# Kernel optimization log

Measured on AMD Instinct MI355X. Metric: run time of the kernel, lower is better.

## Reference

```python
import jax, jax.numpy as jnp
import numpy as np

N = 50000          # nodes
DEG = 16           # out-degree
E = N * DEG        # edges
IN = 256           # input feature dim
H = 8              # hidden heads
DH = 32            # per-head hidden dim (hidden_dim // H)
HID = H * DH       # 256
OUT = 64           # output dim (single output head)
ALPHA = 0.2        # LeakyReLU negative slope


def _xavier(k, shape, fan_in, fan_out):
    limit = 1.414 * np.sqrt(6.0 / (fan_in + fan_out))
    return jax.random.uniform(k, shape, jnp.float32, -limit, limit)


def setup_inputs() -> dict:
    key = jax.random.key(0)
    ks = jax.random.split(key, 6)
    X = jax.random.normal(ks[0], (N, IN), jnp.float32)
    src = jnp.repeat(jnp.arange(N, dtype=jnp.int32), DEG)      # every row non-empty
    dst = jax.random.randint(ks[1], (E,), 0, N, jnp.int32)
    edges = jnp.stack([src, dst])                               # [2, E]
    W0 = _xavier(ks[2], (H, IN, DH), IN, DH)
    a0 = _xavier(ks[3], (H, 2 * DH), 2 * DH, 1)
    W1 = _xavier(ks[4], (1, HID, OUT), HID, OUT)
    a1 = _xavier(ks[5], (1, 2 * OUT), 2 * OUT, 1)
    return {"X": X, "edges": edges, "W0": W0, "a0": a0, "W1": W1, "a1": a1}


def sparse_gat_layer(X, edges, W, a):
    # W: [H, Din, D], a: [H, 2D]. Equivalent to concat(h_src, h_dst) @ a split.
    n = X.shape[0]
    D = W.shape[2]
    src, dst = edges[0], edges[1]
    h = jnp.einsum('nd,hde->hne', X, W)                         # [H, N, D]
    s_src = jnp.einsum('hne,he->hn', h, a[:, :D])               # [H, N]
    s_dst = jnp.einsum('hne,he->hn', h, a[:, D:])               # [H, N]
    e = jax.nn.leaky_relu(s_src[:, src] + s_dst[:, dst], ALPHA)  # [H, E]
    # stable per-row (segment = src) softmax, matching torch.sparse.softmax(dim=1)
    seg_max = jax.lax.stop_gradient(
        jax.vmap(lambda v: jax.ops.segment_max(v, src, num_segments=n))(e))
    p = jnp.exp(e - seg_max[:, src])
    denom = jax.vmap(lambda v: jax.ops.segment_sum(v, src, num_segments=n))(p)
    att = p / denom[:, src]                                      # [H, E]
    # out[i] = sum_{e: src=i} att_e * h[dst_e]
    agg = jax.vmap(lambda a_, hh: jax.ops.segment_sum(a_[:, None] * hh[dst], src,
                                                      num_segments=n))(att, h)
    return agg                                                   # [H, N, D]


def reference(X, edges, W0, a0, W1, a1):
    h1 = jax.nn.elu(sparse_gat_layer(X, edges, W0, a0))          # [H, N, DH]
    X1 = jnp.transpose(h1, (1, 0, 2)).reshape(X.shape[0], -1)    # concat heads [N, HID]
    out = sparse_gat_layer(X1, edges, W1, a1)                    # [1, N, OUT]
    return jax.nn.elu(out[0])                                    # num_heads_out = 1
```

## Files before the change

### kernel.cpp

```cpp
#include <hip/hip_runtime.h>

typedef __attribute__((ext_vector_type(8))) short bh8;
typedef __attribute__((ext_vector_type(4))) float f4;

static __device__ __forceinline__ float b2f(unsigned short u){
  union { unsigned int i; float f; } c; c.i = ((unsigned int)u) << 16; return c.f;
}
static __device__ __forceinline__ unsigned short f2b(float f){
  union { float f; unsigned int i; } c; c.f = f;
  unsigned int u = c.i; u += 0x7fffu + ((u >> 16) & 1u);
  return (unsigned short)(u >> 16);
}
static __device__ __forceinline__ float elu1(float x){ return x > 0.f ? x : (__expf(x) - 1.f); }
static __device__ __forceinline__ float lrelu(float x){ return x > 0.f ? x : 0.2f * x; }
static __device__ __forceinline__ float gload(const void* p, size_t i, int isf32){
  return isf32 ? ((const float*)p)[i] : b2f(((const unsigned short*)p)[i]);
}
static __device__ __forceinline__ int detect_f32(const unsigned int* __restrict__ W0w, int lane){
  unsigned int w = W0w[lane & 63];
  unsigned int e = (w >> 7) & 0xFFu;
  unsigned long long m = __ballot(e >= 100u && e <= 126u);
  return (__popcll(m) < 32) ? 1 : 0;
}

__global__ __launch_bounds__(256) void prep_kernel(
    const void* __restrict__ W0, const void* __restrict__ a0,
    const void* __restrict__ W1, const void* __restrict__ a1,
    unsigned short* __restrict__ Wt1, unsigned short* __restrict__ Wt2){
  int isf = detect_f32((const unsigned int*)W0, threadIdx.x & 63);
  int c = blockIdx.x, k = threadIdx.x;
  if (c < 272){
    float v;
    if (c < 256){
      int h = c >> 5, d = c & 31;
      v = gload(W0, (size_t)(h*256 + k)*32 + d, isf);
    } else if (c < 264){
      int h = c - 256; float s = 0.f;
      for (int d = 0; d < 32; d++)
        s += gload(W0, (size_t)(h*256 + k)*32 + d, isf) * gload(a0, h*64 + d, isf);
      v = s;
    } else {
      int h = c - 264; float s = 0.f;
      for (int d = 0; d < 32; d++)
        s += gload(W0, (size_t)(h*256 + k)*32 + d, isf) * gload(a0, h*64 + 32 + d, isf);
      v = s;
    }
    Wt1[c*256 + k] = f2b(v);
  } else {
    int c2 = c - 272; float v;
    if (c2 < 64) v = gload(W1, k*64 + c2, isf);
    else if (c2 == 64){ float s = 0.f; for (int i = 0; i < 64; i++) s += gload(W1, k*64+i, isf) * gload(a1, i, isf);      v = s; }
    else if (c2 == 65){ float s = 0.f; for (int i = 0; i < 64; i++) s += gload(W1, k*64+i, isf) * gload(a1, 64 + i, isf); v = s; }
    else v = 0.f;
    Wt2[c2*256 + k] = f2b(v);
  }
}

__global__ __launch_bounds__(256, 2) void gemm1_mfma(
    const void* __restrict__ Xraw, const unsigned short* __restrict__ Wt,
    unsigned short* __restrict__ H1, float* __restrict__ S1, int N,
    const void* __restrict__ W0){
  __shared__ __align__(16) unsigned short A[112*264];
  int tid = threadIdx.x, wv = tid >> 6, lane = tid & 63;
  int isf = detect_f32((const unsigned int*)W0, lane);
  int q = lane >> 4, l = lane & 15;
  int n0 = blockIdx.x*112;
  #pragma unroll
  for (int it = 0; it < 14; it++){
    int g = it*256 + tid;
    int r = g >> 5, c = g & 31;
    int grow = n0 + r; if (grow > N-1) grow = N-1;
    bh8 v;
    if (isf){
      const float* xr = (const float*)Xraw + (size_t)grow*256 + c*8;
      float4 u0 = *(const float4*)xr, u1 = *(const float4*)(xr + 4);
      v[0]=(short)f2b(u0.x); v[1]=(short)f2b(u0.y); v[2]=(short)f2b(u0.z); v[3]=(short)f2b(u0.w);
      v[4]=(short)f2b(u1.x); v[5]=(short)f2b(u1.y); v[6]=(short)f2b(u1.z); v[7]=(short)f2b(u1.w);
    } else {
      v = *(const bh8*)((const unsigned short*)Xraw + (size_t)grow*256 + c*8);
    }
    *(bh8*)&A[r*264 + c*8] = v;
  }
  __syncthreads();
  const bh8* Wb = (const bh8*)Wt;
  bh8 B[4][8];
  #pragma unroll
  for (int tt = 0; tt < 4; tt++){
    int t = wv*4 + tt;
    #pragma unroll
    for (int kk = 0; kk < 8; kk++) B[tt][kk] = Wb[(size_t)(t*16 + l)*32 + kk*4 + q];
  }
  for (int m = 0; m < 7; m++){
    bh8 a[8];
    #pragma unroll
    for (int kk = 0; kk < 8; kk++) a[kk] = *(const bh8*)&A[(m*16 + l)*264 + kk*32 + q*8];
    #pragma unroll
    for (int tt = 0; tt < 4; tt++){
      f4 acc = {0.f,0.f,0.f,0.f};
      #pragma unroll
      for (int kk = 0; kk < 8; kk++)
        acc = __builtin_amdgcn_mfma_f32_16x16x32_bf16(a[kk], B[tt][kk], acc, 0, 0, 0);
      int t = wv*4 + tt;
      #pragma unroll
      for (int r = 0; r < 4; r++){
        int row = n0 + m*16 + q*4 + r;
        if (row < N) H1[(size_t)row*256 + t*16 + l] = f2b(acc[r]);
      }
    }
  }
  if (wv == 0){
    bh8 Bs[8];
    #pragma unroll
    for (int kk = 0; kk < 8; kk++) Bs[kk] = Wb[(size_t)(256 + l)*32 + kk*4 + q];
    for (int m = 0; m < 7; m++){
      bh8 a[8];
      #pragma unroll
      for (int kk = 0; kk < 8; kk++) a[kk] = *(const bh8*)&A[(m*16 + l)*264 + kk*32 + q*8];
      f4 acc = {0.f,0.f,0.f,0.f};
      #pragma unroll
      for (int kk = 0; kk < 8; kk++)
        acc = __builtin_amdgcn_mfma_f32_16x16x32_bf16(a[kk], Bs[kk], acc, 0, 0, 0);
      #pragma unroll
      for (int r = 0; r < 4; r++){
        int row = n0 + m*16 + q*4 + r;
        if (row < N) S1[(size_t)row*16 + l] = acc[r];
      }
    }
  }
}

__global__ __launch_bounds__(256) void fused_agg1_gemm2(
    const float* __restrict__ S1, const unsigned short* __restrict__ H1,
    const int* __restrict__ dst, const unsigned short* __restrict__ Wt2,
    unsigned short* __restrict__ H2, float* __restrict__ S2, int N){
  __shared__ __align__(16) unsigned short Xt[32*264];
  __shared__ __align__(16) unsigned short Hs[32*88];
  int tid = threadIdx.x, wv = tid >> 6, lane = tid & 63;
  int n0 = blockIdx.x*32;
  int h = lane >> 3, jj = lane & 7;
  int half = lane >> 5, li = lane & 31;
  int cb = li*8, hc = li >> 2;
  for (int np = 0; np < 4; np++){
    int lrA = wv*8 + np*2, lrB = lrA + 1;
    int nodeA = n0 + lrA; if (nodeA > N-1) nodeA = N-1;
    int nodeB = n0 + lrB; if (nodeB > N-1) nodeB = N-1;
    const int* dpA = dst + (size_t)nodeA*16;
    const int* dpB = dst + (size_t)nodeB*16;
    int d0A = dpA[jj], d1A = dpA[jj + 8];
    int d0B = dpB[jj], d1B = dpB[jj + 8];
    float ssA = S1[(size_t)nodeA*16 + h];
    float ssB = S1[(size_t)nodeB*16 + h];
    float e0A = lrelu(ssA + S1[(size_t)d0A*16 + 8 + h]);
    float e1A = lrelu(ssA + S1[(size_t)d1A*16 + 8 + h]);
    float e0B = lrelu(ssB + S1[(size_t)d0B*16 + 8 + h]);
    float e1B = lrelu(ssB + S1[(size_t)d1B*16 + 8 + h]);
    float mA = fmaxf(e0A, e1A), mB = fmaxf(e0B, e1B);
    mA = fmaxf(mA, __shfl_xor(mA, 1)); mB = fmaxf(mB, __shfl_xor(mB, 1));
    mA = fmaxf(mA, __shfl_xor(mA, 2)); mB = fmaxf(mB, __shfl_xor(mB, 2));
    mA = fmaxf(mA, __shfl_xor(mA, 4)); mB = fmaxf(mB, __shfl_xor(mB, 4));
    float p0A = __expf(e0A - mA), p1A = __expf(e1A - mA);
    float p0B = __expf(e0B - mB), p1B = __expf(e1B - mB);
    float sA = p0A + p1A, sB = p0B + p1B;
    sA += __shfl_xor(sA, 1); sB += __shfl_xor(sB, 1);
    sA += __shfl_xor(sA, 2); sB += __shfl_xor(sB, 2);
    sA += __shfl_xor(sA, 4); sB += __shfl_xor(sB, 4);
    float invA = 1.f / sA, invB = 1.f / sB;
    float v0A = p0A * invA, v1A = p1A * invA;
    float v0B = p0B * invB, v1B = p1B * invB;
    float accA[8] = {0.f,0.f,0.f,0.f,0.f,0.f,0.f,0.f};
    float accB[8] = {0.f,0.f,0.f,0.f,0.f,0.f,0.f,0.f};
    #pragma unroll
    for (int i = 0; i < 8; i++){
      int j  = i*2 + half;
      int jl = j & 7;
      int rowA  = (i < 4) ? __shfl(d0A, jl) : __shfl(d1A, jl);
      int rowB  = (i < 4) ? __shfl(d0B, jl) : __shfl(d1B, jl);
      float awA = (i < 4) ? __shfl(v0A, hc*8 + jl) : __shfl(v1A, hc*8 + jl);
      float awB = (i < 4) ? __shfl(v0B, hc*8 + jl) : __shfl(v1B, hc*8 + jl);
      bh8 vA = *(const bh8*)(H1 + (size_t)rowA*256 + cb);
      bh8 vB = *(const bh8*)(H1 + (size_t)rowB*256 + cb);
      #pragma unroll
      for (int c = 0; c < 8; c++){
        accA[c] += awA * b2f((unsigned short)vA[c]);
        accB[c] += awB * b2f((unsigned short)vB[c]);
      }
    }
    #pragma unroll
    for (int c = 0; c < 8; c++){
      accA[c] += __shfl_xor(accA[c], 32);
      accB[c] += __shfl_xor(accB[c], 32);
    }
    if (half == 0){
      bh8 oA, oB;
      #pragma unroll
      for (int c = 0; c < 8; c++){
        oA[c] = (short)f2b(elu1(accA[c]));
        oB[c] = (short)f2b(elu1(accB[c]));
      }
      *(bh8*)&Xt[lrA*264 + cb] = oA;
      *(bh8*)&Xt[lrB*264 + cb] = oB;
    }
  }
  __syncthreads();
  {
    int q = lane >> 4, l = lane & 15;
    bh8 a0[8], a1[8];
    #pragma unroll
    for (int kk = 0; kk < 8; kk++){
      a0[kk] = *(const bh8*)&Xt[l*264 + kk*32 + q*8];
      a1[kk] = *(const bh8*)&Xt[(16 + l)*264 + kk*32 + q*8];
    }
    const bh8* Wb = (const bh8*)Wt2;
    int ntt = (wv == 3) ? 2 : 1;
    for (int it = 0; it < ntt; it++){
      int tt = (it == 0) ? wv : 4;
      bh8 b[8];
      #pragma unroll
      for (int kk = 0; kk < 8; kk++) b[kk] = Wb[(size_t)(tt*16 + l)*32 + kk*4 + q];
      f4 c0 = {0.f,0.f,0.f,0.f}, c1 = {0.f,0.f,0.f,0.f};
      #pragma unroll
      for (int kk = 0; kk < 8; kk++){
        c0 = __builtin_amdgcn_mfma_f32_16x16x32_bf16(a0[kk], b[kk], c0, 0, 0, 0);
        c1 = __builtin_amdgcn_mfma_f32_16x16x32_bf16(a1[kk], b[kk], c1, 0, 0, 0);
      }
      if (tt < 4){
        #pragma unroll
        for (int r = 0; r < 4; r++){
          Hs[(q*4 + r)*88 + tt*16 + l]      = f2b(c0[r]);
          Hs[(16 + q*4 + r)*88 + tt*16 + l] = f2b(c1[r]);
        }
      } else if (l < 2){
        #pragma unroll
        for (int r = 0; r < 4; r++){
          int row0 = n0 + q*4 + r, row1 = n0 + 16 + q*4 + r;
          if (row0 < N) S2[(size_t)row0*2 + l] = c0[r];
          if (row1 < N) S2[(size_t)row1*2 + l] = c1[r];
        }
      }
    }
  }
  __syncthreads();
  {
    int r2 = tid >> 3, ch = tid & 7;
    int row = n0 + r2;
    if (row < N)
      *(bh8*)(H2 + (size_t)row*64 + ch*8) = *(const bh8*)&Hs[r2*88 + ch*8];
  }
}

__global__ __launch_bounds__(256) void agg2_kernel(
    const float* __restrict__ S2, const unsigned short* __restrict__ H2,
    const int* __restrict__ dst, void* __restrict__ outv, int N,
    const void* __restrict__ W0){
  int tid = threadIdx.x, wv = tid >> 6, lane = tid & 63;
  int isf = detect_f32((const unsigned int*)W0, lane);
  int node = blockIdx.x*4 + wv; if (node > N-1) node = N-1;
  int j = lane & 15;
  int d = dst[(size_t)node*16 + j];
  float e = lrelu(S2[(size_t)node*2] + S2[(size_t)d*2 + 1]);
  float m = e;
  m = fmaxf(m, __shfl_xor(m, 1)); m = fmaxf(m, __shfl_xor(m, 2));
  m = fmaxf(m, __shfl_xor(m, 4)); m = fmaxf(m, __shfl_xor(m, 8));
  float p = __expf(e - m);
  float s = p;
  s += __shfl_xor(s, 1); s += __shfl_xor(s, 2); s += __shfl_xor(s, 4); s += __shfl_xor(s, 8);
  float attv = p / s;
  int g = lane >> 3, cbl = (lane & 7)*8;
  float acc[8] = {0.f,0.f,0.f,0.f,0.f,0.f,0.f,0.f};
  #pragma unroll
  for (int it = 0; it < 2; it++){
    int j2 = it*8 + g;
    float aw = __shfl(attv, j2);
    int row  = __shfl(d,    j2);
    bh8 v = *(const bh8*)(H2 + (size_t)row*64 + cbl);
    #pragma unroll
    for (int c = 0; c < 8; c++) acc[c] += aw * b2f((unsigned short)v[c]);
  }
  #pragma unroll
  for (int c = 0; c < 8; c++){
    acc[c] += __shfl_xor(acc[c], 8);
    acc[c] += __shfl_xor(acc[c], 16);
    acc[c] += __shfl_xor(acc[c], 32);
  }
  if (lane < 8){
    size_t oi = (size_t)node*64 + cbl;
    if (isf){
      float4 f0, f1;
      f0.x = elu1(acc[0]); f0.y = elu1(acc[1]); f0.z = elu1(acc[2]); f0.w = elu1(acc[3]);
      f1.x = elu1(acc[4]); f1.y = elu1(acc[5]); f1.z = elu1(acc[6]); f1.w = elu1(acc[7]);
      *(float4*)((float*)outv + oi)     = f0;
      *(float4*)((float*)outv + oi + 4) = f1;
    } else {
      bh8 o;
      #pragma unroll
      for (int c = 0; c < 8; c++) o[c] = (short)f2b(elu1(acc[c]));
      *(bh8*)((unsigned short*)outv + oi) = o;
    }
  }
}

extern "C" void kernel_launch(void* const* d_in, const int* in_sizes, int n_in,
                              void* d_out, int out_size, void* d_ws, size_t ws_size,
                              hipStream_t stream){
  const void* X  = d_in[0];
  const int*  ed = (const int*)d_in[1];
  const void* W0 = d_in[2];
  const void* a0 = d_in[3];
  const void* W1 = d_in[4];
  const void* a1 = d_in[5];

  int N = in_sizes[0] / 256;
  int E = N * 16;
  const int* dst = ed + E;

  char* w = (char*)d_ws;
  size_t off = 0;
  auto alloc = [&](size_t bytes) -> void* {
    void* p = w + off; off += (bytes + 255) & ~(size_t)255; return p;
  };
  unsigned short* Wt1 = (unsigned short*)alloc(272*256*2);
  unsigned short* Wt2 = (unsigned short*)alloc(80*256*2);
  float*          S1  = (float*)alloc((size_t)N*16*4);
  unsigned short* H1  = (unsigned short*)alloc((size_t)N*256*2);
  unsigned short* H2  = (unsigned short*)alloc((size_t)N*64*2);
  float*          S2  = (float*)alloc((size_t)N*2*4);
  (void)ws_size; (void)n_in; (void)out_size;

  int g1 = (N + 111) / 112;
  int gf = (N + 31) / 32;
  int ab = (N + 3) / 4;
  prep_kernel     <<<352,256, 0, stream>>>(W0, a0, W1, a1, Wt1, Wt2);
  gemm1_mfma      <<<g1, 256, 0, stream>>>(X,  Wt1, H1, S1, N, W0);
  fused_agg1_gemm2<<<gf, 256, 0, stream>>>(S1, H1, dst, Wt2, H2, S2, N);
  agg2_kernel     <<<ab, 256, 0, stream>>>(S2, H2, dst, d_out, N, W0);
}
```

Before: 218.4 us.

## Stage GEMM1 output in LDS for coalesced stores; process two nodes per wave in agg2

In gemm1, the per-element scattered 2-byte stores of H1 are replaced by writing MFMA results back into the shared A tile (after the A fragments are consumed) and then emitting coalesced 16-byte row stores. The separate score-GEMM pass for wave 0 is folded into the main m loop, which reuses the loaded A fragments. agg2 now handles two nodes per wave with interleaved gathers to raise memory-level parallelism, and its grid is halved. The added __syncthreads per m iteration and the extra live registers are the costs.

```diff
diff --git a/kernel.cpp b/kernel.cpp
--- a/kernel.cpp
+++ b/kernel.cpp
@@ -90,42 +90,51 @@
     #pragma unroll
     for (int kk = 0; kk < 8; kk++) B[tt][kk] = Wb[(size_t)(t*16 + l)*32 + kk*4 + q];
   }
+  bh8 Bs[8];
+  if (wv == 0){
+    #pragma unroll
+    for (int kk = 0; kk < 8; kk++) Bs[kk] = Wb[(size_t)(256 + l)*32 + kk*4 + q];
+  }
   for (int m = 0; m < 7; m++){
     bh8 a[8];
     #pragma unroll
     for (int kk = 0; kk < 8; kk++) a[kk] = *(const bh8*)&A[(m*16 + l)*264 + kk*32 + q*8];
+    f4 acc[4];
     #pragma unroll
     for (int tt = 0; tt < 4; tt++){
-      f4 acc = {0.f,0.f,0.f,0.f};
+      f4 z = {0.f,0.f,0.f,0.f}; acc[tt] = z;
       #pragma unroll
       for (int kk = 0; kk < 8; kk++)
-        acc = __builtin_amdgcn_mfma_f32_16x16x32_bf16(a[kk], B[tt][kk], acc, 0, 0, 0);
-      int t = wv*4 + tt;
+        acc[tt] = __builtin_amdgcn_mfma_f32_16x16x32_bf16(a[kk], B[tt][kk], acc[tt], 0, 0, 0);
+    }
+    if (wv == 0){
+      f4 as = {0.f,0.f,0.f,0.f};
+      #pragma unroll
+      for (int kk = 0; kk < 8; kk++)
+        as = __builtin_amdgcn_mfma_f32_16x16x32_bf16(a[kk], Bs[kk], as, 0, 0, 0);
       #pragma unroll
       for (int r = 0; r < 4; r++){
         int row = n0 + m*16 + q*4 + r;
-        if (row < N) H1[(size_t)row*256 + t*16 + l] = f2b(acc[r]);
-      }
-    }
-  }
-  if (wv == 0){
-    bh8 Bs[8];
-    #pragma unroll
-    for (int kk = 0; kk < 8; kk++) Bs[kk] = Wb[(size_t)(256 + l)*32 + kk*4 + q];
-    for (int m = 0; m < 7; m++){
-      bh8 a[8];
-      #pragma unroll
-      for (int kk = 0; kk < 8; kk++) a[kk] = *(const bh8*)&A[(m*16 + l)*264 + kk*32 + q*8];
-      f4 acc = {0.f,0.f,0.f,0.f};
-      #pragma unroll
-      for (int kk = 0; kk < 8; kk++)
-        acc = __builtin_amdgcn_mfma_f32_16x16x32_bf16(a[kk], Bs[kk], acc, 0, 0, 0);
-      #pragma unroll
-      for (int r = 0; r < 4; r++){
-        int row = n0 + m*16 + q*4 + r;
-        if (row < N) S1[(size_t)row*16 + l] = acc[r];
-      }
-    }
+        if (row < N) S1[(size_t)row*16 + l] = as[r];
+      }
+    }
+    __syncthreads();
+    #pragma unroll
+    for (int tt = 0; tt < 4; tt++){
+      int t = wv*4 + tt;
+      #pragma unroll
+      for (int r = 0; r < 4; r++)
+        A[(m*16 + q*4 + r)*264 + t*16 + l] = f2b(acc[tt][r]);
+    }
+    __syncthreads();
+  }
+  #pragma unroll
+  for (int g = 0; g < 14; g++){
+    int idx = g*256 + tid;
+    int r = idx >> 5, c = idx & 31;
+    int row = n0 + r;
+    if (row < N)
+      *(bh8*)(H1 + (size_t)row*256 + c*8) = *(const bh8*)&A[r*264 + c*8];
   }
 }
 
@@ -254,47 +263,69 @@
     const void* __restrict__ W0){
   int tid = threadIdx.x, wv = tid >> 6, lane = tid & 63;
   int isf = detect_f32((const unsigned int*)W0, lane);
-  int node = blockIdx.x*4 + wv; if (node > N-1) node = N-1;
+  int nodeA = blockIdx.x*8 + wv*2; if (nodeA > N-1) nodeA = N-1;
+  int nodeB = nodeA + 1;           if (nodeB > N-1) nodeB = N-1;
   int j = lane & 15;
-  int d = dst[(size_t)node*16 + j];
-  float e = lrelu(S2[(size_t)node*2] + S2[(size_t)d*2 + 1]);
-  float m = e;
-  m = fmaxf(m, __shfl_xor(m, 1)); m = fmaxf(m, __shfl_xor(m, 2));
-  m = fmaxf(m, __shfl_xor(m, 4)); m = fmaxf(m, __shfl_xor(m, 8));
-  float p = __expf(e - m);
-  float s = p;
-  s += __shfl_xor(s, 1); s += __shfl_xor(s, 2); s += __shfl_xor(s, 4); s += __shfl_xor(s, 8);
-  float attv = p / s;
+  int dA = dst[(size_t)nodeA*16 + j];
+  int dB = dst[(size_t)nodeB*16 + j];
+  float eA = lrelu(S2[(size_t)nodeA*2] + S2[(size_t)dA*2 + 1]);
+  float eB = lrelu(S2[(size_t)nodeB*2] + S2[(size_t)dB*2 + 1]);
+  float mA = eA, mB = eB;
+  mA = fmaxf(mA, __shfl_xor(mA, 1)); mB = fmaxf(mB, __shfl_xor(mB, 1));
+  mA = fmaxf(mA, __shfl_xor(mA, 2)); mB = fmaxf(mB, __shfl_xor(mB, 2));
+  mA = fmaxf(mA, __shfl_xor(mA, 4)); mB = fmaxf(mB, __shfl_xor(mB, 4));
+  mA = fmaxf(mA, __shfl_xor(mA, 8)); mB = fmaxf(mB, __shfl_xor(mB, 8));
+  float pA = __expf(eA - mA), pB = __expf(eB - mB);
+  float sA = pA, sB = pB;
+  sA += __shfl_xor(sA, 1); sB += __shfl_xor(sB, 1);
+  sA += __shfl_xor(sA, 2); sB += __shfl_xor(sB, 2);
+  sA += __shfl_xor(sA, 4); sB += __shfl_xor(sB, 4);
+  sA += __shfl_xor(sA, 8); sB += __shfl_xor(sB, 8);
+  float attA = pA / sA, attB = pB / sB;
   int g = lane >> 3, cbl = (lane & 7)*8;
-  float acc[8] = {0.f,0.f,0.f,0.f,0.f,0.f,0.f,0.f};
+  float accA[8] = {0.f,0.f,0.f,0.f,0.f,0.f,0.f,0.f};
+  float accB[8] = {0.f,0.f,0.f,0.f,0.f,0.f,0.f,0.f};
   #pragma unroll
   for (int it = 0; it < 2; it++){
     int j2 = it*8 + g;
-    float aw = __shfl(attv, j2);
-    int row  = __shfl(d,    j2);
-    bh8 v = *(const bh8*)(H2 + (size_t)row*64 + cbl);
-    #pragma unroll
-    for (int c = 0; c < 8; c++) acc[c] += aw * b2f((unsigned short)v[c]);
+    float awA = __shfl(attA, j2), awB = __shfl(attB, j2);
+    int rowA  = __shfl(dA,   j2), rowB  = __shfl(dB,   j2);
+    bh8 vA = *(const bh8*)(H2 + (size_t)rowA*64 + cbl);
+    bh8 vB = *(const bh8*)(H2 + (size_t)rowB*64 + cbl);
+    #pragma unroll
+    for (int c = 0; c < 8; c++){
+      accA[c] += awA * b2f((unsigned short)vA[c]);
+      accB[c] += awB * b2f((unsigned short)vB[c]);
+    }
   }
   #pragma unroll
   for (int c = 0; c < 8; c++){
-    acc[c] += __shfl_xor(acc[c], 8);
-    acc[c] += __shfl_xor(acc[c], 16);
-    acc[c] += __shfl_xor(acc[c], 32);
+    accA[c] += __shfl_xor(accA[c], 8);  accB[c] += __shfl_xor(accB[c], 8);
+    accA[c] += __shfl_xor(accA[c], 16); accB[c] += __shfl_xor(accB[c], 16);
+    accA[c] += __shfl_xor(accA[c], 32); accB[c] += __shfl_xor(accB[c], 32);
   }
   if (lane < 8){
-    size_t oi = (size_t)node*64 + cbl;
+    size_t oiA = (size_t)nodeA*64 + cbl;
+    size_t oiB = (size_t)nodeB*64 + cbl;
     if (isf){
-      float4 f0, f1;
-      f0.x = elu1(acc[0]); f0.y = elu1(acc[1]); f0.z = elu1(acc[2]); f0.w = elu1(acc[3]);
-      f1.x = elu1(acc[4]); f1.y = elu1(acc[5]); f1.z = elu1(acc[6]); f1.w = elu1(acc[7]);
-      *(float4*)((float*)outv + oi)     = f0;
-      *(float4*)((float*)outv + oi + 4) = f1;
+      float4 a0v, a1v, b0v, b1v;
+      a0v.x = elu1(accA[0]); a0v.y = elu1(accA[1]); a0v.z = elu1(accA[2]); a0v.w = elu1(accA[3]);
+      a1v.x = elu1(accA[4]); a1v.y = elu1(accA[5]); a1v.z = elu1(accA[6]); a1v.w = elu1(accA[7]);
+      b0v.x = elu1(accB[0]); b0v.y = elu1(accB[1]); b0v.z = elu1(accB[2]); b0v.w = elu1(accB[3]);
+      b1v.x = elu1(accB[4]); b1v.y = elu1(accB[5]); b1v.z = elu1(accB[6]); b1v.w = elu1(accB[7]);
+      *(float4*)((float*)outv + oiA)     = a0v;
+      *(float4*)((float*)outv + oiA + 4) = a1v;
+      *(float4*)((float*)outv + oiB)     = b0v;
+      *(float4*)((float*)outv + oiB + 4) = b1v;
     } else {
-      bh8 o;
-      #pragma unroll
-      for (int c = 0; c < 8; c++) o[c] = (short)f2b(elu1(acc[c]));
-      *(bh8*)((unsigned short*)outv + oi) = o;
+      bh8 oA, oB;
+      #pragma unroll
+      for (int c = 0; c < 8; c++){
+        oA[c] = (short)f2b(elu1(accA[c]));
+        oB[c] = (short)f2b(elu1(accB[c]));
+      }
+      *(bh8*)((unsigned short*)outv + oiA) = oA;
+      *(bh8*)((unsigned short*)outv + oiB) = oB;
     }
   }
 }
@@ -328,7 +359,7 @@
 
   int g1 = (N + 111) / 112;
   int gf = (N + 31) / 32;
-  int ab = (N + 3) / 4;
+  int ab = (N + 7) / 8;
   prep_kernel     <<<352,256, 0, stream>>>(W0, a0, W1, a1, Wt1, Wt2);
   gemm1_mfma      <<<g1, 256, 0, stream>>>(X,  Wt1, H1, S1, N, W0);
   fused_agg1_gemm2<<<gf, 256, 0, stream>>>(S1, H1, dst, Wt2, H2, S2, N);
```

After: 215.4 us. No clear change (-1.4%).
